# Optimization experiments

Measured on AMD Instinct MI355X. Metric: run time of the kernel, lower is better.

Reference implementation:

```python
import jax, jax.numpy as jnp
import numpy as np

NUM_TIMES = 1024  # times are drawn from [0, 1024), used as fixed segment count
N = 16777216


def setup_inputs() -> dict:
    key = jax.random.key(0)
    k1, k2, k3 = jax.random.split(key, 3)
    outs = jax.random.normal(k1, (N,), dtype=jnp.float32)
    T_E = jax.random.randint(k2, (N,), 0, 2, dtype=jnp.int32)
    T_T = jax.random.randint(k3, (N,), 0, NUM_TIMES, dtype=jnp.int32)
    return {"outs": outs, "T_E": T_E, "T_T": T_T}


def reference(outs, T_E, T_T):
    # E[E > 0] = 1  -> binary event indicator
    E = (T_E > 0).astype(outs.dtype)
    # Y_label_T = |T_T| ; integer times act directly as segment ids
    seg_ids = jnp.abs(T_T)
    Obs = jnp.sum(E)
    # log of running sum of hazards: log(cumsum(exp(yhat)))
    y_hat_cumsum = jnp.log(jnp.cumsum(jnp.exp(outs)))
    # original segment_max initializes accumulator at 0, so it is clipped below at 0;
    # jnp.maximum also neutralizes -inf fill for empty segments (count=0 there anyway)
    seg_max = jnp.maximum(
        jax.ops.segment_max(y_hat_cumsum, seg_ids, num_segments=NUM_TIMES), 0.0
    )
    seg_cnt = jax.ops.segment_sum(E, seg_ids, num_segments=NUM_TIMES)
    loss_s2 = jnp.sum(seg_max * seg_cnt)
    loss_s1 = jnp.sum(outs * E)
    return (loss_s2 - loss_s1) / Obs
```

## Files before the change

### kernel.cpp

```cpp
#include <hip/hip_runtime.h>

#define NUM_SEGS 1024
#define CHUNK_LOG 13
#define CHUNK (1 << CHUNK_LOG)
#define SUBCH 4
#define SUPER (CHUNK * SUBCH)
#define BLK 1024
#define NWAVE (BLK / 64)
#define SEGBLK 256

__device__ __forceinline__ float waveReduceSumF(float v) {
#pragma unroll
    for (int off = 32; off > 0; off >>= 1) v += __shfl_down(v, off, 64);
    return v;
}
__device__ __forceinline__ double waveReduceSumD(double v) {
#pragma unroll
    for (int off = 32; off > 0; off >>= 1) v += __shfl_down(v, off, 64);
    return v;
}
__device__ __forceinline__ unsigned waveReduceSumU(unsigned v) {
#pragma unroll
    for (int off = 32; off > 0; off >>= 1) v += __shfl_down(v, off, 64);
    return v;
}
__device__ __forceinline__ int waveReduceMaxI(int v) {
#pragma unroll
    for (int off = 32; off > 0; off >>= 1) {
        const int o = __shfl_down(v, off, 64);
        v = o > v ? o : v;
    }
    return v;
}

__global__ void init_kernel(unsigned* __restrict__ seg_cnt,
                            int* __restrict__ last_chunk,
                            unsigned* __restrict__ obs,
                            double* __restrict__ loss1,
                            double* __restrict__ loss2,
                            unsigned* __restrict__ done) {
    const int t = blockIdx.x * blockDim.x + threadIdx.x;
    if (t < NUM_SEGS) { seg_cnt[t] = 0u; last_chunk[t] = -1; }
    if (t == 0) { obs[0] = 0u; loss1[0] = 0.0; loss2[0] = 0.0; done[0] = 0u; }
}

__global__ __launch_bounds__(BLK, 8) void pass1_kernel(
    const float* __restrict__ outs, const int* __restrict__ te,
    const int* __restrict__ tt, int N, int nChunks,
    float* __restrict__ chunk_sums, unsigned* __restrict__ seg_cnt,
    int* __restrict__ last_chunk, unsigned* __restrict__ obs,
    double* __restrict__ loss1) {
    __shared__ unsigned hist[NUM_SEGS];
    __shared__ unsigned char flags[NUM_SEGS];
    __shared__ float redF[NWAVE];
    __shared__ unsigned redU[NWAVE];

    for (int t = threadIdx.x; t < NUM_SEGS; t += BLK) hist[t] = 0u;
    if (threadIdx.x < NUM_SEGS / 4)
        reinterpret_cast<unsigned*>(flags)[threadIdx.x] = 0xFFFFFFFFu;
    __syncthreads();

    float sumOE = 0.f;
    unsigned cntE = 0u;
    const int superBase = blockIdx.x * SUPER;
    const int lane = threadIdx.x & 63;
    const int wid = threadIdx.x >> 6;

#pragma unroll 1
    for (int k = 0; k < SUBCH; ++k) {
        const int cbase = superBase + k * CHUNK;
        float sumExp = 0.f;
        if (cbase + CHUNK <= N) {
#pragma unroll
            for (int it = 0; it < CHUNK / (BLK * 4); ++it) {
                const int i = cbase + it * (BLK * 4) + (threadIdx.x << 2);
                const float4 o = *reinterpret_cast<const float4*>(outs + i);
                const int4 ev = *reinterpret_cast<const int4*>(te + i);
                const int4 sv = *reinterpret_cast<const int4*>(tt + i);
                const float e0 = __expf(o.x), e1 = __expf(o.y);
                const float e2 = __expf(o.z), e3 = __expf(o.w);
                sumExp += (e0 + e1) + (e2 + e3);
                const int s0 = sv.x < 0 ? -sv.x : sv.x;
                const int s1 = sv.y < 0 ? -sv.y : sv.y;
                const int s2 = sv.z < 0 ? -sv.z : sv.z;
                const int s3 = sv.w < 0 ? -sv.w : sv.w;
                flags[s0] = (unsigned char)k;
                flags[s1] = (unsigned char)k;
                flags[s2] = (unsigned char)k;
                flags[s3] = (unsigned char)k;
                if (ev.x > 0) { cntE++; sumOE += o.x; atomicAdd(&hist[s0], 1u); }
                if (ev.y > 0) { cntE++; sumOE += o.y; atomicAdd(&hist[s1], 1u); }
                if (ev.z > 0) { cntE++; sumOE += o.z; atomicAdd(&hist[s2], 1u); }
                if (ev.w > 0) { cntE++; sumOE += o.w; atomicAdd(&hist[s3], 1u); }
            }
        } else {
            const int end = (cbase + CHUNK < N) ? cbase + CHUNK : N;
            for (int i = cbase + (int)threadIdx.x; i < end; i += BLK) {
                const float o = outs[i];
                const int e = te[i];
                int s = tt[i]; s = s < 0 ? -s : s;
                sumExp += __expf(o);
                flags[s] = (unsigned char)k;
                if (e > 0) { cntE++; sumOE += o; atomicAdd(&hist[s], 1u); }
            }
        }
        const float w = waveReduceSumF(sumExp);
        if (lane == 0) redF[wid] = w;
        __syncthreads();
        if (threadIdx.x == 0) {
            float s4 = 0.f;
#pragma unroll
            for (int j = 0; j < NWAVE; ++j) s4 += redF[j];
            const int cidx = cbase >> CHUNK_LOG;
            if (cidx < nChunks) chunk_sums[cidx] = s4;
        }
        __syncthreads();
    }

    const int chunk0 = blockIdx.x * SUBCH;
    for (int t = threadIdx.x; t < NUM_SEGS; t += BLK) {
        const unsigned h = hist[t];
        if (h) atomicAdd(&seg_cnt[t], h);
        const unsigned f = flags[t];
        if (f != 0xFFu) atomicMax(&last_chunk[t], chunk0 + (int)f);
    }

    const float wOE = waveReduceSumF(sumOE);
    const unsigned wC = waveReduceSumU(cntE);
    if (lane == 0) { redF[wid] = wOE; redU[wid] = wC; }
    __syncthreads();
    if (threadIdx.x == 0) {
        float oe = 0.f; unsigned c = 0u;
#pragma unroll
        for (int j = 0; j < NWAVE; ++j) { oe += redF[j]; c += redU[j]; }
        atomicAdd(loss1, (double)oe);
        atomicAdd(obs, c);
    }
}

__global__ __launch_bounds__(SEGBLK) void seg_final_kernel(
    const float* __restrict__ outs, const int* __restrict__ tt,
    const float* __restrict__ csums, const unsigned* __restrict__ seg_cnt,
    const int* __restrict__ last_chunk, const double* __restrict__ loss1,
    double* __restrict__ loss2, const unsigned* __restrict__ obs,
    unsigned* __restrict__ done, float* __restrict__ out, int N) {
    __shared__ double redD[SEGBLK / 64];
    __shared__ float redF[SEGBLK / 64];
    __shared__ int redI[SEGBLK / 64];
    __shared__ int s_li;

    const int t = blockIdx.x;
    const unsigned cnt = seg_cnt[t];
    const int lane = threadIdx.x & 63, wid = threadIdx.x >> 6;

    if (cnt != 0u) {
        const int lc = last_chunk[t];
        double p = 0.0;
        for (int c = threadIdx.x; c < lc; c += SEGBLK) p += (double)csums[c];
        p = waveReduceSumD(p);
        if (lane == 0) redD[wid] = p;

        const int base = lc << CHUNK_LOG;
        const int end = (base + CHUNK < N) ? base + CHUNK : N;
        int li = -1;
        for (int i = base + (int)threadIdx.x; i < end; i += SEGBLK) {
            int s = tt[i]; s = s < 0 ? -s : s;
            if (s == t) li = i;
        }
        li = waveReduceMaxI(li);
        if (lane == 0) redI[wid] = li;
        __syncthreads();
        if (threadIdx.x == 0) {
            int m = redI[0];
#pragma unroll
            for (int j = 1; j < SEGBLK / 64; ++j) m = redI[j] > m ? redI[j] : m;
            s_li = m;
        }
        __syncthreads();
        const int LI = s_li;

        float fs = 0.f;
        for (int i = base + (int)threadIdx.x; i <= LI; i += SEGBLK) fs += __expf(outs[i]);
        fs = waveReduceSumF(fs);
        if (lane == 0) redF[wid] = fs;
        __syncthreads();
        if (threadIdx.x == 0 && LI >= 0) {
            double pre = 0.0;
            float fsum = 0.f;
#pragma unroll
            for (int j = 0; j < SEGBLK / 64; ++j) { pre += redD[j]; fsum += redF[j]; }
            double sm = log(pre + (double)fsum);
            if (sm < 0.0) sm = 0.0;
            atomicAdd(loss2, sm * (double)cnt);
        }
    }

    if (threadIdx.x == 0) {
        __threadfence();
        const unsigned d = atomicAdd(done, 1u);
        if (d == (unsigned)(gridDim.x - 1)) {
            const double l2 = atomicAdd(loss2, 0.0);
            const double l1 = loss1[0];
            const unsigned o = obs[0];
            out[0] = (float)((l2 - l1) / (double)o);
        }
    }
}

extern "C" void kernel_launch(void* const* d_in, const int* in_sizes, int n_in,
                              void* d_out, int out_size, void* d_ws, size_t ws_size,
                              hipStream_t stream) {
    const float* outs = (const float*)d_in[0];
    const int* te = (const int*)d_in[1];
    const int* tt = (const int*)d_in[2];
    const int N = in_sizes[0];
    float* out = (float*)d_out;

    const int nChunks = (N + CHUNK - 1) / CHUNK;

    char* ws = (char*)d_ws;
    double* d_loss1 = (double*)ws;
    double* d_loss2 = d_loss1 + 1;
    float* d_csums = (float*)(ws + 16);
    unsigned* d_segcnt = (unsigned*)(d_csums + nChunks);
    int* d_lastchunk = (int*)(d_segcnt + NUM_SEGS);
    unsigned* d_obs = (unsigned*)(d_lastchunk + NUM_SEGS);
    unsigned* d_done = d_obs + 1;

    init_kernel<<<(NUM_SEGS + 255) / 256, 256, 0, stream>>>(
        d_segcnt, d_lastchunk, d_obs, d_loss1, d_loss2, d_done);
    const int nSuper = (N + SUPER - 1) / SUPER;
    pass1_kernel<<<nSuper, BLK, 0, stream>>>(outs, te, tt, N, nChunks, d_csums,
                                             d_segcnt, d_lastchunk, d_obs, d_loss1);
    seg_final_kernel<<<NUM_SEGS, SEGBLK, 0, stream>>>(
        outs, tt, d_csums, d_segcnt, d_lastchunk, d_loss1, d_loss2, d_obs, d_done,
        out, N);
}
```

Baseline: 240.0 us.

## Drop per-segment last-chunk tracking; search backward from final chunk in finalizer

Pass 1 no longer writes per-element shared flags or does global atomicMax for each segment's last chunk, and it drops the per-chunk block barriers. Per-chunk exp sums are kept in registers and combined with per-wave float atomics into zero-initialized chunk sums. The block size drops to 512 and the loop is fully unrolled. The finalizer instead scans chunks backward from the end with vectorized int4 loads to find each segment's last occurrence, which usually hits in the final chunk for dense segments. The cost is a slower worst case for sparse segments and atomic ordering nondeterminism in the chunk sums.

```diff
diff --git a/kernel.cpp b/kernel.cpp
--- a/kernel.cpp
+++ b/kernel.cpp
@@ -5,7 +5,7 @@
 #define CHUNK (1 << CHUNK_LOG)
 #define SUBCH 4
 #define SUPER (CHUNK * SUBCH)
-#define BLK 1024
+#define BLK 512
 #define NWAVE (BLK / 64)
 #define SEGBLK 256
 
@@ -34,95 +34,87 @@
 }
 
 __global__ void init_kernel(unsigned* __restrict__ seg_cnt,
-                            int* __restrict__ last_chunk,
+                            float* __restrict__ csums, int nChunks,
                             unsigned* __restrict__ obs,
                             double* __restrict__ loss1,
                             double* __restrict__ loss2,
                             unsigned* __restrict__ done) {
     const int t = blockIdx.x * blockDim.x + threadIdx.x;
-    if (t < NUM_SEGS) { seg_cnt[t] = 0u; last_chunk[t] = -1; }
+    if (t < NUM_SEGS) seg_cnt[t] = 0u;
+    if (t < nChunks) csums[t] = 0.f;
     if (t == 0) { obs[0] = 0u; loss1[0] = 0.0; loss2[0] = 0.0; done[0] = 0u; }
 }
 
-__global__ __launch_bounds__(BLK, 8) void pass1_kernel(
+__global__ __launch_bounds__(BLK, 4) void pass1_kernel(
     const float* __restrict__ outs, const int* __restrict__ te,
     const int* __restrict__ tt, int N, int nChunks,
-    float* __restrict__ chunk_sums, unsigned* __restrict__ seg_cnt,
-    int* __restrict__ last_chunk, unsigned* __restrict__ obs,
-    double* __restrict__ loss1) {
+    float* __restrict__ csums, unsigned* __restrict__ seg_cnt,
+    unsigned* __restrict__ obs, double* __restrict__ loss1) {
     __shared__ unsigned hist[NUM_SEGS];
-    __shared__ unsigned char flags[NUM_SEGS];
     __shared__ float redF[NWAVE];
     __shared__ unsigned redU[NWAVE];
 
     for (int t = threadIdx.x; t < NUM_SEGS; t += BLK) hist[t] = 0u;
-    if (threadIdx.x < NUM_SEGS / 4)
-        reinterpret_cast<unsigned*>(flags)[threadIdx.x] = 0xFFFFFFFFu;
     __syncthreads();
 
+    const int lane = threadIdx.x & 63;
+    const int wid = threadIdx.x >> 6;
+    const int superBase = blockIdx.x * SUPER;
+
+    float sE[SUBCH] = {0.f, 0.f, 0.f, 0.f};
     float sumOE = 0.f;
     unsigned cntE = 0u;
-    const int superBase = blockIdx.x * SUPER;
-    const int lane = threadIdx.x & 63;
-    const int wid = threadIdx.x >> 6;
-
-#pragma unroll 1
-    for (int k = 0; k < SUBCH; ++k) {
-        const int cbase = superBase + k * CHUNK;
-        float sumExp = 0.f;
-        if (cbase + CHUNK <= N) {
-#pragma unroll
-            for (int it = 0; it < CHUNK / (BLK * 4); ++it) {
-                const int i = cbase + it * (BLK * 4) + (threadIdx.x << 2);
-                const float4 o = *reinterpret_cast<const float4*>(outs + i);
-                const int4 ev = *reinterpret_cast<const int4*>(te + i);
-                const int4 sv = *reinterpret_cast<const int4*>(tt + i);
-                const float e0 = __expf(o.x), e1 = __expf(o.y);
-                const float e2 = __expf(o.z), e3 = __expf(o.w);
-                sumExp += (e0 + e1) + (e2 + e3);
-                const int s0 = sv.x < 0 ? -sv.x : sv.x;
-                const int s1 = sv.y < 0 ? -sv.y : sv.y;
-                const int s2 = sv.z < 0 ? -sv.z : sv.z;
-                const int s3 = sv.w < 0 ? -sv.w : sv.w;
-                flags[s0] = (unsigned char)k;
-                flags[s1] = (unsigned char)k;
-                flags[s2] = (unsigned char)k;
-                flags[s3] = (unsigned char)k;
-                if (ev.x > 0) { cntE++; sumOE += o.x; atomicAdd(&hist[s0], 1u); }
-                if (ev.y > 0) { cntE++; sumOE += o.y; atomicAdd(&hist[s1], 1u); }
-                if (ev.z > 0) { cntE++; sumOE += o.z; atomicAdd(&hist[s2], 1u); }
-                if (ev.w > 0) { cntE++; sumOE += o.w; atomicAdd(&hist[s3], 1u); }
-            }
-        } else {
+
+    if (superBase + SUPER <= N) {
+#pragma unroll
+        for (int u = 0; u < SUBCH * 4; ++u) {
+            const int k = u >> 2, it = u & 3;
+            const int i = superBase + (k << CHUNK_LOG) + (wid << 10) + (it << 8) +
+                          (lane << 2);
+            const float4 o = *reinterpret_cast<const float4*>(outs + i);
+            const int4 ev = *reinterpret_cast<const int4*>(te + i);
+            const int4 sv = *reinterpret_cast<const int4*>(tt + i);
+            const float e0 = __expf(o.x), e1 = __expf(o.y);
+            const float e2 = __expf(o.z), e3 = __expf(o.w);
+            sE[k] += (e0 + e1) + (e2 + e3);
+            const int s0 = sv.x < 0 ? -sv.x : sv.x;
+            const int s1 = sv.y < 0 ? -sv.y : sv.y;
+            const int s2 = sv.z < 0 ? -sv.z : sv.z;
+            const int s3 = sv.w < 0 ? -sv.w : sv.w;
+            if (ev.x > 0) { cntE++; sumOE += o.x; atomicAdd(&hist[s0], 1u); }
+            if (ev.y > 0) { cntE++; sumOE += o.y; atomicAdd(&hist[s1], 1u); }
+            if (ev.z > 0) { cntE++; sumOE += o.z; atomicAdd(&hist[s2], 1u); }
+            if (ev.w > 0) { cntE++; sumOE += o.w; atomicAdd(&hist[s3], 1u); }
+        }
+    } else {
+        for (int k = 0; k < SUBCH; ++k) {
+            const int cbase = superBase + k * CHUNK;
+            if (cbase >= N) break;
             const int end = (cbase + CHUNK < N) ? cbase + CHUNK : N;
             for (int i = cbase + (int)threadIdx.x; i < end; i += BLK) {
                 const float o = outs[i];
                 const int e = te[i];
                 int s = tt[i]; s = s < 0 ? -s : s;
-                sumExp += __expf(o);
-                flags[s] = (unsigned char)k;
+                sE[k] += __expf(o);
                 if (e > 0) { cntE++; sumOE += o; atomicAdd(&hist[s], 1u); }
             }
         }
-        const float w = waveReduceSumF(sumExp);
-        if (lane == 0) redF[wid] = w;
-        __syncthreads();
-        if (threadIdx.x == 0) {
-            float s4 = 0.f;
-#pragma unroll
-            for (int j = 0; j < NWAVE; ++j) s4 += redF[j];
-            const int cidx = cbase >> CHUNK_LOG;
-            if (cidx < nChunks) chunk_sums[cidx] = s4;
-        }
-        __syncthreads();
-    }
-
-    const int chunk0 = blockIdx.x * SUBCH;
+    }
+
+#pragma unroll
+    for (int k = 0; k < SUBCH; ++k) {
+        const float w = waveReduceSumF(sE[k]);
+        if (lane == 0) {
+            const int cidx = (superBase >> CHUNK_LOG) + k;
+            if (cidx < nChunks) atomicAdd(&csums[cidx], w);
+        }
+    }
+
+    __syncthreads();
+
     for (int t = threadIdx.x; t < NUM_SEGS; t += BLK) {
         const unsigned h = hist[t];
         if (h) atomicAdd(&seg_cnt[t], h);
-        const unsigned f = flags[t];
-        if (f != 0xFFu) atomicMax(&last_chunk[t], chunk0 + (int)f);
     }
 
     const float wOE = waveReduceSumF(sumOE);
@@ -141,9 +133,9 @@
 __global__ __launch_bounds__(SEGBLK) void seg_final_kernel(
     const float* __restrict__ outs, const int* __restrict__ tt,
     const float* __restrict__ csums, const unsigned* __restrict__ seg_cnt,
-    const int* __restrict__ last_chunk, const double* __restrict__ loss1,
-    double* __restrict__ loss2, const unsigned* __restrict__ obs,
-    unsigned* __restrict__ done, float* __restrict__ out, int N) {
+    const double* __restrict__ loss1, double* __restrict__ loss2,
+    const unsigned* __restrict__ obs, unsigned* __restrict__ done,
+    float* __restrict__ out, int N, int nChunks) {
     __shared__ double redD[SEGBLK / 64];
     __shared__ float redF[SEGBLK / 64];
     __shared__ int redI[SEGBLK / 64];
@@ -154,44 +146,66 @@
     const int lane = threadIdx.x & 63, wid = threadIdx.x >> 6;
 
     if (cnt != 0u) {
-        const int lc = last_chunk[t];
-        double p = 0.0;
-        for (int c = threadIdx.x; c < lc; c += SEGBLK) p += (double)csums[c];
-        p = waveReduceSumD(p);
-        if (lane == 0) redD[wid] = p;
-
-        const int base = lc << CHUNK_LOG;
-        const int end = (base + CHUNK < N) ? base + CHUNK : N;
-        int li = -1;
-        for (int i = base + (int)threadIdx.x; i < end; i += SEGBLK) {
-            int s = tt[i]; s = s < 0 ? -s : s;
-            if (s == t) li = i;
-        }
-        li = waveReduceMaxI(li);
-        if (lane == 0) redI[wid] = li;
-        __syncthreads();
-        if (threadIdx.x == 0) {
-            int m = redI[0];
-#pragma unroll
-            for (int j = 1; j < SEGBLK / 64; ++j) m = redI[j] > m ? redI[j] : m;
-            s_li = m;
-        }
-        __syncthreads();
-        const int LI = s_li;
-
-        float fs = 0.f;
-        for (int i = base + (int)threadIdx.x; i <= LI; i += SEGBLK) fs += __expf(outs[i]);
-        fs = waveReduceSumF(fs);
-        if (lane == 0) redF[wid] = fs;
-        __syncthreads();
-        if (threadIdx.x == 0 && LI >= 0) {
-            double pre = 0.0;
-            float fsum = 0.f;
-#pragma unroll
-            for (int j = 0; j < SEGBLK / 64; ++j) { pre += redD[j]; fsum += redF[j]; }
-            double sm = log(pre + (double)fsum);
-            if (sm < 0.0) sm = 0.0;
-            atomicAdd(loss2, sm * (double)cnt);
+        int c = nChunks - 1;
+        int LI = -1;
+        for (;;) {
+            const int base = c << CHUNK_LOG;
+            const int end = (base + CHUNK < N) ? base + CHUNK : N;
+            const int span = end - base;
+            const int qspan = span & ~3;
+            int li = -1;
+            for (int i = base + ((int)threadIdx.x << 2); i < base + qspan;
+                 i += SEGBLK * 4) {
+                const int4 sv = *reinterpret_cast<const int4*>(tt + i);
+                const int s0 = sv.x < 0 ? -sv.x : sv.x;
+                const int s1 = sv.y < 0 ? -sv.y : sv.y;
+                const int s2 = sv.z < 0 ? -sv.z : sv.z;
+                const int s3 = sv.w < 0 ? -sv.w : sv.w;
+                if (s3 == t) li = i + 3;
+                else if (s2 == t) li = i + 2;
+                else if (s1 == t) li = i + 1;
+                else if (s0 == t) li = i;
+            }
+            for (int i = base + qspan + (int)threadIdx.x; i < end; i += SEGBLK) {
+                int s = tt[i]; s = s < 0 ? -s : s;
+                if (s == t && i > li) li = i;
+            }
+            li = waveReduceMaxI(li);
+            if (lane == 0) redI[wid] = li;
+            __syncthreads();
+            if (threadIdx.x == 0) {
+                int m = redI[0];
+#pragma unroll
+                for (int j = 1; j < SEGBLK / 64; ++j) m = redI[j] > m ? redI[j] : m;
+                s_li = m;
+            }
+            __syncthreads();
+            LI = s_li;
+            if (LI >= 0 || --c < 0) break;
+        }
+
+        if (LI >= 0) {
+            double p = 0.0;
+            for (int j = threadIdx.x; j < c; j += SEGBLK) p += (double)csums[j];
+            p = waveReduceSumD(p);
+            if (lane == 0) redD[wid] = p;
+
+            const int base = c << CHUNK_LOG;
+            float fs = 0.f;
+            for (int i = base + (int)threadIdx.x; i <= LI; i += SEGBLK)
+                fs += __expf(outs[i]);
+            fs = waveReduceSumF(fs);
+            if (lane == 0) redF[wid] = fs;
+            __syncthreads();
+            if (threadIdx.x == 0) {
+                double pre = 0.0;
+                float fsum = 0.f;
+#pragma unroll
+                for (int j = 0; j < SEGBLK / 64; ++j) { pre += redD[j]; fsum += redF[j]; }
+                double sm = log(pre + (double)fsum);
+                if (sm < 0.0) sm = 0.0;
+                atomicAdd(loss2, sm * (double)cnt);
+            }
         }
     }
 
@@ -200,8 +214,8 @@
         const unsigned d = atomicAdd(done, 1u);
         if (d == (unsigned)(gridDim.x - 1)) {
             const double l2 = atomicAdd(loss2, 0.0);
-            const double l1 = loss1[0];
-            const unsigned o = obs[0];
+            const double l1 = *(volatile const double*)loss1;
+            const unsigned o = *(volatile const unsigned*)obs;
             out[0] = (float)((l2 - l1) / (double)o);
         }
     }
@@ -223,16 +237,16 @@
     double* d_loss2 = d_loss1 + 1;
     float* d_csums = (float*)(ws + 16);
     unsigned* d_segcnt = (unsigned*)(d_csums + nChunks);
-    int* d_lastchunk = (int*)(d_segcnt + NUM_SEGS);
-    unsigned* d_obs = (unsigned*)(d_lastchunk + NUM_SEGS);
+    unsigned* d_obs = d_segcnt + NUM_SEGS;
     unsigned* d_done = d_obs + 1;
 
-    init_kernel<<<(NUM_SEGS + 255) / 256, 256, 0, stream>>>(
-        d_segcnt, d_lastchunk, d_obs, d_loss1, d_loss2, d_done);
+    const int initThreads = (nChunks > NUM_SEGS ? nChunks : NUM_SEGS);
+    init_kernel<<<(initThreads + 255) / 256, 256, 0, stream>>>(
+        d_segcnt, d_csums, nChunks, d_obs, d_loss1, d_loss2, d_done);
     const int nSuper = (N + SUPER - 1) / SUPER;
     pass1_kernel<<<nSuper, BLK, 0, stream>>>(outs, te, tt, N, nChunks, d_csums,
-                                             d_segcnt, d_lastchunk, d_obs, d_loss1);
+                                             d_segcnt, d_obs, d_loss1);
     seg_final_kernel<<<NUM_SEGS, SEGBLK, 0, stream>>>(
-        outs, tt, d_csums, d_segcnt, d_lastchunk, d_loss1, d_loss2, d_obs, d_done,
-        out, N);
-}
+        outs, tt, d_csums, d_segcnt, d_loss1, d_loss2, d_obs, d_done, out, N,
+        nChunks);
+}
```

Result: slower. 249.2 us (+3.8%).
